# Performance work log

Measured on AMD Instinct MI355X. Metric: run time of the kernel, lower is better.

The kernel has to match this reference:

```python
import jax, jax.numpy as jnp
from jax import lax
import numpy as np

VOCAB, EMB, HID, B, T = 500, 64, 64, 512, 512


def setup_inputs() -> dict:
    key = jax.random.key(0)
    ks = jax.random.split(key, 12)
    s_ih = 1.0 / np.sqrt(HID)
    emb = jax.random.normal(ks[0], (VOCAB, EMB), dtype=jnp.float32)
    emb = emb.at[0].set(0.0)  # padding_idx=0 row is zero-initialized
    u = lambda k, shape: jax.random.uniform(k, shape, jnp.float32, -s_ih, s_ih)
    return {
        "x": jax.random.randint(ks[1], (B, T), 0, VOCAB, dtype=jnp.int64),
        "emb": emb,
        "W_ih0": u(ks[2], (HID, EMB)), "W_hh0": u(ks[3], (HID, HID)),
        "b_ih0": u(ks[4], (HID,)),     "b_hh0": u(ks[5], (HID,)),
        "W_ih1": u(ks[6], (HID, HID)), "W_hh1": u(ks[7], (HID, HID)),
        "b_ih1": u(ks[8], (HID,)),     "b_hh1": u(ks[9], (HID,)),
        "fc_w": u(ks[10], (1, HID)),   "fc_b": u(ks[11], (1,)),
    }


def reference(x, emb, W_ih0, W_hh0, b_ih0, b_hh0, W_ih1, W_hh1, b_ih1, b_hh1, fc_w, fc_b):
    e = emb[x]                                        # [B,T,EMB]
    # Layer-0 input projection is time-parallel; precompute as one big GEMM.
    xin0 = jnp.einsum('bte,he->bth', e, W_ih0) + b_ih0  # [B,T,HID]

    def step(carry, xt):
        h1, h2 = carry
        h1 = jnp.tanh(xt + h1 @ W_hh0.T + b_hh0)
        h2 = jnp.tanh(h1 @ W_ih1.T + b_ih1 + h2 @ W_hh1.T + b_hh1)
        return (h1, h2), None

    h0 = jnp.zeros((x.shape[0], HID), dtype=e.dtype)
    (h1, h2), _ = lax.scan(step, (h0, h0), jnp.swapaxes(xin0, 0, 1))  # scan over T
    return h2 @ fc_w.T + fc_b                          # [B,1]
```

## Files before the change

kernel.cpp:

```cpp
#include <hip/hip_runtime.h>
#include <math.h>

#define VOCAB 500
#define EMB   64
#define HID   64
#define BB    512
#define TT    512
#define KC    8
#define NC    (TT / KC)

__device__ __forceinline__ float fast_tanh(float x) {
    float ax = fabsf(x);
    float e  = __expf(-2.0f * ax);
    float r  = __builtin_amdgcn_rcpf(1.0f + e);
    float t  = fmaf(-2.0f * e, r, 1.0f);
    return copysignf(t, x);
}

__device__ __forceinline__ float bcast(float v, int lane) {
    return __int_as_float(__builtin_amdgcn_readlane(__float_as_int(v), lane));
}

__global__ __launch_bounds__(64) void proj_kernel(
        const float* __restrict__ emb,
        const float* __restrict__ W_ih0,
        const float* __restrict__ b_ih0,
        float* __restrict__ proj) {
    const int v = blockIdx.x;
    const int j = threadIdx.x;
    const float4* e4 = (const float4*)(emb + v * EMB);
    const float4* w4 = (const float4*)(W_ih0 + j * EMB);
    float acc = b_ih0[j];
    #pragma unroll
    for (int k = 0; k < EMB / 4; ++k) {
        float4 e = e4[k];
        float4 w = w4[k];
        acc = fmaf(w.x, e.x, acc);
        acc = fmaf(w.y, e.y, acc);
        acc = fmaf(w.z, e.z, acc);
        acc = fmaf(w.w, e.w, acc);
    }
    proj[v * HID + j] = acc;
}

__global__ __launch_bounds__(256, 1) void rnn_kernel(
        const int*   __restrict__ x,
        const float* __restrict__ proj,
        const float* __restrict__ W_hh0,
        const float* __restrict__ b_hh0,
        const float* __restrict__ W_ih1,
        const float* __restrict__ W_hh1,
        const float* __restrict__ b_ih1,
        const float* __restrict__ b_hh1,
        const float* __restrict__ fc_w,
        const float* __restrict__ fc_b,
        float* __restrict__ out) {
    const int b   = blockIdx.x;
    const int tid = threadIdx.x;
    const int wid = tid >> 6;
    const int j   = tid & 63;

    __shared__ __align__(16) float H1R[2][KC][HID];
    __shared__ __align__(16) float AAa[2][KC][HID];
    __shared__ __align__(16) float AAb[2][KC][HID];
    __shared__ int xls[TT];

    for (int t = tid; t < TT; t += 256) xls[t] = x[b * TT + t];

    const float* wsrc =
        (wid == 0) ? (W_hh0 + j * HID) :
        (wid == 3) ? (W_hh1 + j * HID) : (W_ih1 + j * HID);
    float w[HID];
    {
        const float4* w4 = (const float4*)wsrc;
        #pragma unroll
        for (int k = 0; k < HID / 4; ++k) {
            float4 t4 = w4[k];
            w[4*k+0] = t4.x; w[4*k+1] = t4.y; w[4*k+2] = t4.z; w[4*k+3] = t4.w;
        }
    }
    #pragma unroll
    for (int k = 0; k < HID; ++k) asm volatile("" : "+v"(w[k]));

    const float bh0 = b_hh0[j];
    const float bi1 = b_ih1[j] + b_hh1[j];
    const float fcw = fc_w[j];

    __syncthreads();

    float h1reg = 0.0f, h2reg = 0.0f;
    float xin[KC], xinN[KC];
    if (wid == 0) {
        #pragma unroll
        for (int u = 0; u < KC; ++u) xin[u] = proj[xls[u] * HID + j];
    }

    for (int c = 0; c < NC + 2; ++c) {
        if (wid == 0) {
            if (c < NC) {
                const int base = ((c + 1) & (NC - 1)) * KC;
                #pragma unroll
                for (int u = 0; u < KC; ++u)
                    xinN[u] = proj[xls[base + u] * HID + j];

                #pragma unroll
                for (int u = 0; u < KC; ++u) {
                    float a0 = xin[u] + bh0, a1 = 0.0f, a2 = 0.0f, a3 = 0.0f;
                    #pragma unroll
                    for (int k = 0; k < HID; k += 4) {
                        a0 = fmaf(w[k+0], bcast(h1reg, k+0), a0);
                        a1 = fmaf(w[k+1], bcast(h1reg, k+1), a1);
                        a2 = fmaf(w[k+2], bcast(h1reg, k+2), a2);
                        a3 = fmaf(w[k+3], bcast(h1reg, k+3), a3);
                    }
                    h1reg = fast_tanh((a0 + a1) + (a2 + a3));
                    H1R[c & 1][u][j] = h1reg;
                    xin[u] = xinN[u];
                }
            }
        } else if (wid == 1) {
            if (c >= 1 && c <= NC) {
                const int p = (c - 1) & 1;
                #pragma unroll
                for (int u = 0; u < KC; ++u) {
                    const float4* hv = (const float4*)(&H1R[p][u][0]);
                    float a0 = 0.0f, a1 = 0.0f, a2 = 0.0f, a3 = 0.0f;
                    #pragma unroll
                    for (int k = 0; k < 8; ++k) {
                        float4 h = hv[k];
                        a0 = fmaf(w[4*k+0], h.x, a0);
                        a1 = fmaf(w[4*k+1], h.y, a1);
                        a2 = fmaf(w[4*k+2], h.z, a2);
                        a3 = fmaf(w[4*k+3], h.w, a3);
                    }
                    AAa[p][u][j] = (a0 + a1) + (a2 + a3);
                }
            }
        } else if (wid == 2) {
            if (c >= 1 && c <= NC) {
                const int p = (c - 1) & 1;
                #pragma unroll
                for (int u = 0; u < KC; ++u) {
                    const float4* hv = (const float4*)(&H1R[p][u][0]);
                    float a0 = 0.0f, a1 = 0.0f, a2 = 0.0f, a3 = 0.0f;
                    #pragma unroll
                    for (int k = 8; k < 16; ++k) {
                        float4 h = hv[k];
                        a0 = fmaf(w[4*k+0], h.x, a0);
                        a1 = fmaf(w[4*k+1], h.y, a1);
                        a2 = fmaf(w[4*k+2], h.z, a2);
                        a3 = fmaf(w[4*k+3], h.w, a3);
                    }
                    AAb[p][u][j] = (a0 + a1) + (a2 + a3);
                }
            }
        } else {
            if (c >= 2) {
                const int p = c & 1;
                #pragma unroll
                for (int u = 0; u < KC; ++u) {
                    float a0 = (AAa[p][u][j] + AAb[p][u][j]) + bi1;
                    float a1 = 0.0f, a2 = 0.0f, a3 = 0.0f;
                    #pragma unroll
                    for (int k = 0; k < HID; k += 4) {
                        a0 = fmaf(w[k+0], bcast(h2reg, k+0), a0);
                        a1 = fmaf(w[k+1], bcast(h2reg, k+1), a1);
                        a2 = fmaf(w[k+2], bcast(h2reg, k+2), a2);
                        a3 = fmaf(w[k+3], bcast(h2reg, k+3), a3);
                    }
                    h2reg = fast_tanh((a0 + a1) + (a2 + a3));
                }
            }
        }
        __syncthreads();
    }

    if (wid == 3) {
        float val = h2reg * fcw;
        #pragma unroll
        for (int o = 32; o > 0; o >>= 1) val += __shfl_down(val, o, 64);
        if (j == 0) out[b] = val + fc_b[0];
    }
}

extern "C" void kernel_launch(void* const* d_in, const int* in_sizes, int n_in,
                              void* d_out, int out_size, void* d_ws, size_t ws_size,
                              hipStream_t stream) {
    const int*   x     = (const int*)  d_in[0];
    const float* emb   = (const float*)d_in[1];
    const float* W_ih0 = (const float*)d_in[2];
    const float* W_hh0 = (const float*)d_in[3];
    const float* b_ih0 = (const float*)d_in[4];
    const float* b_hh0 = (const float*)d_in[5];
    const float* W_ih1 = (const float*)d_in[6];
    const float* W_hh1 = (const float*)d_in[7];
    const float* b_ih1 = (const float*)d_in[8];
    const float* b_hh1 = (const float*)d_in[9];
    const float* fc_w  = (const float*)d_in[10];
    const float* fc_b  = (const float*)d_in[11];
    float* out  = (float*)d_out;
    float* proj = (float*)d_ws;

    proj_kernel<<<VOCAB, 64, 0, stream>>>(emb, W_ih0, b_ih0, proj);
    rnn_kernel<<<BB, 256, 0, stream>>>(x, proj, W_hh0, b_hh0,
                                       W_ih1, W_hh1, b_ih1, b_hh1,
                                       fc_w, fc_b, out);
}
```

Before: 305.8 us.

## Split two-layer RNN into separate per-layer kernels via global intermediate buffer

```diff
diff --git a/kernel.cpp b/kernel.cpp
--- a/kernel.cpp
+++ b/kernel.cpp
@@ -43,7 +43,159 @@
     proj[v * HID + j] = acc;
 }
 
-__global__ __launch_bounds__(256, 1) void rnn_kernel(
+__global__ __launch_bounds__(64, 1) void h1_kernel(
+        const int*   __restrict__ x,
+        const float* __restrict__ proj,
+        const float* __restrict__ W_hh0,
+        const float* __restrict__ b_hh0,
+        const float* __restrict__ W_ih1,
+        float* __restrict__ Aout) {
+    const int b = blockIdx.x;
+    const int j = threadIdx.x;
+
+    __shared__ __align__(16) float hbuf[HID];
+    __shared__ int xls[TT];
+
+    for (int t = j; t < TT; t += 64) xls[t] = x[b * TT + t];
+
+    float w0[HID], w1[HID];
+    {
+        const float4* a4 = (const float4*)(W_hh0 + j * HID);
+        const float4* c4 = (const float4*)(W_ih1 + j * HID);
+        #pragma unroll
+        for (int k = 0; k < HID / 4; ++k) {
+            float4 t0 = a4[k];
+            w0[4*k+0] = t0.x; w0[4*k+1] = t0.y; w0[4*k+2] = t0.z; w0[4*k+3] = t0.w;
+            float4 t1 = c4[k];
+            w1[4*k+0] = t1.x; w1[4*k+1] = t1.y; w1[4*k+2] = t1.z; w1[4*k+3] = t1.w;
+        }
+    }
+    #pragma unroll
+    for (int k = 0; k < HID; ++k) asm volatile("" : "+v"(w0[k]), "+v"(w1[k]));
+
+    const float bh0 = b_hh0[j];
+    hbuf[j] = 0.0f;
+    __syncthreads();
+
+    float xin[KC], xinN[KC];
+    #pragma unroll
+    for (int u = 0; u < KC; ++u) xin[u] = proj[xls[u] * HID + j];
+
+    float* Arow = Aout + (size_t)b * TT * HID;
+
+    for (int c = 0; c < NC; ++c) {
+        const int base = ((c + 1) & (NC - 1)) * KC;
+        #pragma unroll
+        for (int u = 0; u < KC; ++u)
+            xinN[u] = proj[xls[base + u] * HID + j];
+
+        #pragma unroll
+        for (int u = 0; u < KC; ++u) {
+            const int t = c * KC + u;
+            const float4* hv = (const float4*)hbuf;
+            float a0 = xin[u] + bh0, a1 = 0.0f, a2 = 0.0f, a3 = 0.0f;
+            float p0 = 0.0f, p1 = 0.0f, p2 = 0.0f, p3 = 0.0f;
+            #pragma unroll
+            for (int k = 0; k < HID / 4; ++k) {
+                float4 h = hv[k];
+                a0 = fmaf(w0[4*k+0], h.x, a0);
+                a1 = fmaf(w0[4*k+1], h.y, a1);
+                a2 = fmaf(w0[4*k+2], h.z, a2);
+                a3 = fmaf(w0[4*k+3], h.w, a3);
+                p0 = fmaf(w1[4*k+0], h.x, p0);
+                p1 = fmaf(w1[4*k+1], h.y, p1);
+                p2 = fmaf(w1[4*k+2], h.z, p2);
+                p3 = fmaf(w1[4*k+3], h.w, p3);
+            }
+            const float h1n = fast_tanh((a0 + a1) + (a2 + a3));
+            if (t > 0) Arow[(t - 1) * HID + j] = (p0 + p1) + (p2 + p3);
+            hbuf[j] = h1n;
+            xin[u] = xinN[u];
+        }
+    }
+    {
+        const float4* hv = (const float4*)hbuf;
+        float p0 = 0.0f, p1 = 0.0f, p2 = 0.0f, p3 = 0.0f;
+        #pragma unroll
+        for (int k = 0; k < HID / 4; ++k) {
+            float4 h = hv[k];
+            p0 = fmaf(w1[4*k+0], h.x, p0);
+            p1 = fmaf(w1[4*k+1], h.y, p1);
+            p2 = fmaf(w1[4*k+2], h.z, p2);
+            p3 = fmaf(w1[4*k+3], h.w, p3);
+        }
+        Arow[(TT - 1) * HID + j] = (p0 + p1) + (p2 + p3);
+    }
+}
+
+__global__ __launch_bounds__(64, 1) void h2_kernel(
+        const float* __restrict__ A,
+        const float* __restrict__ W_hh1,
+        const float* __restrict__ b_ih1,
+        const float* __restrict__ b_hh1,
+        const float* __restrict__ fc_w,
+        const float* __restrict__ fc_b,
+        float* __restrict__ out) {
+    const int b = blockIdx.x;
+    const int j = threadIdx.x;
+
+    __shared__ __align__(16) float hbuf[HID];
+
+    float w[HID];
+    {
+        const float4* a4 = (const float4*)(W_hh1 + j * HID);
+        #pragma unroll
+        for (int k = 0; k < HID / 4; ++k) {
+            float4 t0 = a4[k];
+            w[4*k+0] = t0.x; w[4*k+1] = t0.y; w[4*k+2] = t0.z; w[4*k+3] = t0.w;
+        }
+    }
+    #pragma unroll
+    for (int k = 0; k < HID; ++k) asm volatile("" : "+v"(w[k]));
+
+    const float bi1 = b_ih1[j] + b_hh1[j];
+    const float fcw = fc_w[j];
+    const float* Arow = A + (size_t)b * TT * HID;
+
+    hbuf[j] = 0.0f;
+    __syncthreads();
+
+    float ain[KC], ainN[KC];
+    #pragma unroll
+    for (int u = 0; u < KC; ++u) ain[u] = Arow[u * HID + j];
+
+    float h2n = 0.0f;
+    for (int c = 0; c < NC; ++c) {
+        const int base = ((c + 1) & (NC - 1)) * KC;
+        #pragma unroll
+        for (int u = 0; u < KC; ++u)
+            ainN[u] = Arow[(base + u) * HID + j];
+
+        #pragma unroll
+        for (int u = 0; u < KC; ++u) {
+            const float4* hv = (const float4*)hbuf;
+            float a0 = ain[u] + bi1, a1 = 0.0f, a2 = 0.0f, a3 = 0.0f;
+            #pragma unroll
+            for (int k = 0; k < HID / 4; ++k) {
+                float4 h = hv[k];
+                a0 = fmaf(w[4*k+0], h.x, a0);
+                a1 = fmaf(w[4*k+1], h.y, a1);
+                a2 = fmaf(w[4*k+2], h.z, a2);
+                a3 = fmaf(w[4*k+3], h.w, a3);
+            }
+            h2n = fast_tanh((a0 + a1) + (a2 + a3));
+            hbuf[j] = h2n;
+            ain[u] = ainN[u];
+        }
+    }
+
+    float val = h2n * fcw;
+    #pragma unroll
+    for (int o = 32; o > 0; o >>= 1) val += __shfl_down(val, o, 64);
+    if (j == 0) out[b] = val + fc_b[0];
+}
+
+__global__ __launch_bounds__(256, 1) void rnn_fallback(
         const int*   __restrict__ x,
         const float* __restrict__ proj,
         const float* __restrict__ W_hh0,
@@ -102,7 +254,6 @@
                 #pragma unroll
                 for (int u = 0; u < KC; ++u)
                     xinN[u] = proj[xls[base + u] * HID + j];
-
                 #pragma unroll
                 for (int u = 0; u < KC; ++u) {
                     float a0 = xin[u] + bh0, a1 = 0.0f, a2 = 0.0f, a3 = 0.0f;
@@ -199,10 +350,22 @@
     const float* fc_w  = (const float*)d_in[10];
     const float* fc_b  = (const float*)d_in[11];
     float* out  = (float*)d_out;
+
     float* proj = (float*)d_ws;
+    const size_t projB = (size_t)VOCAB * HID * sizeof(float);
+    const size_t padB  = (256 - (projB & 255)) & 255;
+    float* Abuf = (float*)((char*)d_ws + projB + padB);
+    const size_t needB = projB + padB + (size_t)BB * TT * HID * sizeof(float);
 
     proj_kernel<<<VOCAB, 64, 0, stream>>>(emb, W_ih0, b_ih0, proj);
-    rnn_kernel<<<BB, 256, 0, stream>>>(x, proj, W_hh0, b_hh0,
-                                       W_ih1, W_hh1, b_ih1, b_hh1,
-                                       fc_w, fc_b, out);
-}
+
+    if (ws_size >= needB) {
+        h1_kernel<<<BB, 64, 0, stream>>>(x, proj, W_hh0, b_hh0, W_ih1, Abuf);
+        h2_kernel<<<BB, 64, 0, stream>>>(Abuf, W_hh1, b_ih1, b_hh1,
+                                         fc_w, fc_b, out);
+    } else {
+        rnn_fallback<<<BB, 256, 0, stream>>>(x, proj, W_hh0, b_hh0,
+                                             W_ih1, W_hh1, b_ih1, b_hh1,
+                                             fc_w, fc_b, out);
+    }
+}
```

New measurement: 455.3 us. 1.49x slower.
